# Kernel tuning notes

Measured on AMD Instinct MI355X. Metric: run time of the kernel, lower is better.

Reference implementation:

```python
import jax, jax.numpy as jnp
import numpy as np

EMB = 192
HEADS = 6
WIN = (8, 8)
N = WIN[0] * WIN[1]  # 64
B_ = 2048
NW = 1024  # mask windows per image; B_ % NW == 0


def _relative_position_index():
    coords_h = np.arange(WIN[0])
    coords_w = np.arange(WIN[1])
    coords = np.stack(np.meshgrid(coords_h, coords_w, indexing='ij'))  # (2,Wh,Ww)
    cf = coords.reshape(2, -1)
    rel = cf[:, :, None] - cf[:, None, :]  # (2,N,N)
    rel = rel.transpose(1, 2, 0)
    rel[:, :, 0] += WIN[0] - 1
    rel[:, :, 1] += WIN[1] - 1
    rel[:, :, 0] *= 2 * WIN[1] - 1
    return rel.sum(-1).astype(np.int32)  # (N,N)


def setup_inputs() -> dict:
    key = jax.random.key(0)
    ks = jax.random.split(key, 12)
    num_bias = (2 * WIN[0] - 1) * (2 * WIN[1] - 1)  # 225
    s = 0.02
    return {
        'q': jax.random.normal(ks[0], (B_, N, EMB), jnp.float32),
        'k': jax.random.normal(ks[1], (B_, N, EMB), jnp.float32),
        'v': jax.random.normal(ks[2], (B_, N, EMB), jnp.float32),
        'mask': jax.random.normal(ks[3], (NW, N, N), jnp.float32),
        'Wq': jax.random.normal(ks[4], (EMB, EMB), jnp.float32) * s,
        'bq': jnp.zeros((EMB,), jnp.float32),
        'Wk': jax.random.normal(ks[5], (EMB, EMB), jnp.float32) * s,
        'bk': jnp.zeros((EMB,), jnp.float32),
        'Wv': jax.random.normal(ks[6], (EMB, EMB), jnp.float32) * s,
        'bv': jnp.zeros((EMB,), jnp.float32),
        'Wp': jax.random.normal(ks[7], (EMB, EMB), jnp.float32) * s,
        'bp': jnp.zeros((EMB,), jnp.float32),
        'bias_table': jax.random.normal(ks[8], (num_bias, HEADS), jnp.float32) * s,
        'rel_index': jnp.asarray(_relative_position_index()),
    }


def reference(q, k, v, mask, Wq, bq, Wk, bk, Wv, bv, Wp, bp, bias_table, rel_index):
    head_dim = EMB // HEADS
    scale = head_dim ** -0.5

    def split_heads(x):
        # (B_,N,C) -> (B_,H,N,D)
        return x.reshape(B_, N, HEADS, head_dim).transpose(0, 2, 1, 3)

    qh = split_heads(q @ Wq + bq) * scale
    kh = split_heads(k @ Wk + bk)
    vh = split_heads(v @ Wv + bv)

    attn = jnp.einsum('bhnd,bhmd->bhnm', qh, kh)  # (B_,H,N,N)

    # gathered relative position bias: (N,N,H) -> (H,N,N)
    rel_bias = bias_table[rel_index.reshape(-1)].reshape(N, N, HEADS).transpose(2, 0, 1)
    attn = attn + rel_bias[None]

    # mask add: reshape to (B, nW, H, N, N) and broadcast mask over batch/heads
    nW = mask.shape[0]
    attn = attn.reshape(-1, nW, HEADS, N, N) + mask[None, :, None]
    attn = attn.reshape(-1, HEADS, N, N)
    attn = jax.nn.softmax(attn, axis=-1)

    x = jnp.einsum('bhnm,bhmd->bhnd', attn, vh)  # (B_,H,N,D)
    x = x.transpose(0, 2, 1, 3).reshape(B_, N, EMB)
    x = x @ Wp + bp
    return (x, attn)
```

## Files before the change

kernel.cpp:

```cpp
#include <hip/hip_runtime.h>
#include <hip/hip_bf16.h>

typedef __attribute__((ext_vector_type(8))) short   bf16x8;
typedef __attribute__((ext_vector_type(4))) float   f32x4;
typedef unsigned short u16;

#define NTOK 64
#define CEMB 192
#define NH   6
#define ROWB 384
#define VROWB 128

__device__ __forceinline__ u16 f2b(float f) {
  unsigned u = __float_as_uint(f);
  unsigned r = (u + 0x7fffu + ((u >> 16) & 1u)) >> 16;
  return (u16)r;
}

__device__ __forceinline__ unsigned cvtpk(float lo, float hi) {
  unsigned r;
  asm("v_cvt_pk_bf16_f32 %0, %1, %2" : "=v"(r) : "v"(lo), "v"(hi));
  return r;
}

__device__ __forceinline__ int swz(int row, int colbyte) {
  return colbyte ^ ((((row >> 3) ^ row) & 7) << 4);
}

__global__ void prep_kernel(const float* __restrict__ Wq, const float* __restrict__ Wk,
                            const float* __restrict__ Wv, const float* __restrict__ Wp,
                            const float* __restrict__ btab, const int* __restrict__ ridx,
                            u16* __restrict__ WT, float* __restrict__ rb) {
  int idx = blockIdx.x * 256 + threadIdx.x;
  if (idx < 4 * 36864) {
    int m = idx / 36864;
    int e = idx - m * 36864;
    int n = e / CEMB;
    int k = e - n * CEMB;
    const float* W = (m == 0) ? Wq : (m == 1) ? Wk : (m == 2) ? Wv : Wp;
    WT[idx] = f2b(W[k * CEMB + n]);
  } else {
    int i2 = idx - 4 * 36864;
    if (i2 < NH * 4096) {
      int h = i2 >> 12;
      int ij = i2 & 4095;
      rb[i2] = btab[ridx[ij] * NH + h];
    }
  }
}

__global__ __launch_bounds__(512, 4)
void wattn_kernel(const float* __restrict__ qg, const float* __restrict__ kg,
                  const float* __restrict__ vg, const float* __restrict__ maskg,
                  const float* __restrict__ bq, const float* __restrict__ bk,
                  const float* __restrict__ bv, const float* __restrict__ bp,
                  const u16* __restrict__ WT, const float* __restrict__ rb,
                  float* __restrict__ xout, float* __restrict__ attn_out) {
  __shared__ __align__(16) char smem[81920];
  char* sQ = smem;
  char* sK = smem + 24576;
  char* sV = smem + 49152;
  const int tid  = threadIdx.x;
  const int wave = tid >> 6;
  const int lane = tid & 63;
  const int l15  = lane & 15;
  const int lhi  = lane >> 4;
  char* sP = smem + 73728 + wave * 1024;
  const int b = blockIdx.x;
  const float scale = 0.17677669529663687f;

  {
    const size_t base = (size_t)b * NTOK * CEMB;
    #pragma unroll
    for (int m = 0; m < 3; ++m) {
      const float* src = (m == 0 ? qg : m == 1 ? kg : vg) + base;
      char* dst = (m == 0 ? sQ : m == 1 ? sK : sV);
      #pragma unroll
      for (int it = 0; it < 6; ++it) {
        int fi  = it * 512 + tid;
        int row = fi / 48;
        int ce  = (fi - row * 48) * 4;
        const float4 v4 = reinterpret_cast<const float4*>(src)[fi];
        uint2 w;
        w.x = cvtpk(v4.x, v4.y);
        w.y = cvtpk(v4.z, v4.w);
        *reinterpret_cast<uint2*>(dst + row * ROWB + swz(row, ce * 2)) = w;
      }
    }
  }
  __syncthreads();

  #pragma unroll
  for (int m = 0; m < 3; ++m) {
    const char* Xs = (m == 0) ? sQ : (m == 1) ? sK : sV;
    const float* bias = (m == 0) ? bq : (m == 1) ? bk : bv;
    f32x4 acc[2][4];
    #pragma unroll
    for (int si = 0; si < 2; ++si) {
      int strip = wave + si * 8;
      if (strip < 12) {
        const u16* Wt = WT + m * 36864 + (strip * 16 + l15) * CEMB + lhi * 8;
        #pragma unroll
        for (int rt = 0; rt < 4; ++rt) { f32x4 z = {0.f,0.f,0.f,0.f}; acc[si][rt] = z; }
        #pragma unroll
        for (int ks = 0; ks < 6; ++ks) {
          bf16x8 bw = *reinterpret_cast<const bf16x8*>(Wt + ks * 32);
          #pragma unroll
          for (int rt = 0; rt < 4; ++rt) {
            int row = rt * 16 + l15;
            bf16x8 ax = *reinterpret_cast<const bf16x8*>(Xs + row * ROWB + swz(row, ks * 64 + lhi * 16));
            acc[si][rt] = __builtin_amdgcn_mfma_f32_16x16x32_bf16(ax, bw, acc[si][rt], 0, 0, 0);
          }
        }
      }
    }
    __syncthreads();
    #pragma unroll
    for (int si = 0; si < 2; ++si) {
      int strip = wave + si * 8;
      if (strip < 12) {
        int c = strip * 16 + l15;
        float bval = bias[c];
        if (m == 0) {
          #pragma unroll
          for (int rt = 0; rt < 4; ++rt)
            #pragma unroll
            for (int r = 0; r < 4; ++r) {
              int row = rt * 16 + lhi * 4 + r;
              *reinterpret_cast<u16*>(sQ + row * ROWB + swz(row, c * 2)) = f2b((acc[si][rt][r] + bval) * scale);
            }
        } else if (m == 1) {
          #pragma unroll
          for (int rt = 0; rt < 4; ++rt)
            #pragma unroll
            for (int r = 0; r < 4; ++r) {
              int row = rt * 16 + lhi * 4 + r;
              *reinterpret_cast<u16*>(sK + row * ROWB + swz(row, c * 2)) = f2b(acc[si][rt][r] + bval);
            }
        } else {
          #pragma unroll
          for (int rt = 0; rt < 4; ++rt) {
            int t0 = rt * 16 + lhi * 4;
            uint2 w;
            w.x = cvtpk(acc[si][rt][0] + bval, acc[si][rt][1] + bval);
            w.y = cvtpk(acc[si][rt][2] + bval, acc[si][rt][3] + bval);
            *reinterpret_cast<uint2*>(sV + c * VROWB + swz(c, t0 * 2)) = w;
          }
        }
      }
    }
  }
  __syncthreads();

  const float* maskw = maskg + (size_t)(b & 1023) * 4096;
  const int rt   = wave & 3;
  const int irow = rt * 16 + lhi * 4;

  const float* mkp = maskw + irow * 64 + l15;
  float mkv[4][4];
  #pragma unroll
  for (int ct = 0; ct < 4; ++ct)
    #pragma unroll
    for (int r = 0; r < 4; ++r)
      mkv[ct][r] = mkp[r * 64 + ct * 16];

  #pragma unroll
  for (int ui = 0; ui < 3; ++ui) {
    int u = wave + ui * 8;
    int h = u >> 2;

    const float* rbp = rb + h * 4096 + irow * 64 + l15;
    float rbv[4][4];
    #pragma unroll
    for (int ct = 0; ct < 4; ++ct)
      #pragma unroll
      for (int r = 0; r < 4; ++r)
        rbv[ct][r] = rbp[r * 64 + ct * 16];

    int qrow = rt * 16 + l15;
    bf16x8 aq = *reinterpret_cast<const bf16x8*>(sQ + qrow * ROWB + swz(qrow, h * 64 + lhi * 16));
    f32x4 sv[4];
    #pragma unroll
    for (int ct = 0; ct < 4; ++ct) {
      int krow = ct * 16 + l15;
      bf16x8 bkf = *reinterpret_cast<const bf16x8*>(sK + krow * ROWB + swz(krow, h * 64 + lhi * 16));
      f32x4 z = {0.f, 0.f, 0.f, 0.f};
      sv[ct] = __builtin_amdgcn_mfma_f32_16x16x32_bf16(aq, bkf, z, 0, 0, 0);
    }

    float lg[4][4];
    #pragma unroll
    for (int ct = 0; ct < 4; ++ct)
      #pragma unroll
      for (int r = 0; r < 4; ++r)
        lg[ct][r] = sv[ct][r] + rbv[ct][r] + mkv[ct][r];

    float pr[4][4];
    #pragma unroll
    for (int r = 0; r < 4; ++r) {
      float mx = fmaxf(fmaxf(lg[0][r], lg[1][r]), fmaxf(lg[2][r], lg[3][r]));
      mx = fmaxf(mx, __shfl_xor(mx, 1));
      mx = fmaxf(mx, __shfl_xor(mx, 2));
      mx = fmaxf(mx, __shfl_xor(mx, 4));
      mx = fmaxf(mx, __shfl_xor(mx, 8));
      float e0 = __expf(lg[0][r] - mx), e1 = __expf(lg[1][r] - mx);
      float e2 = __expf(lg[2][r] - mx), e3 = __expf(lg[3][r] - mx);
      float sum = e0 + e1 + e2 + e3;
      sum += __shfl_xor(sum, 1);
      sum += __shfl_xor(sum, 2);
      sum += __shfl_xor(sum, 4);
      sum += __shfl_xor(sum, 8);
      float inv = 1.0f / sum;
      pr[0][r] = e0 * inv; pr[1][r] = e1 * inv; pr[2][r] = e2 * inv; pr[3][r] = e3 * inv;
    }

    float* ap = attn_out + (((size_t)b * NH + h) * NTOK + irow) * NTOK;
    #pragma unroll
    for (int ct = 0; ct < 4; ++ct)
      #pragma unroll
      for (int r = 0; r < 4; ++r)
        ap[r * 64 + ct * 16 + l15] = pr[ct][r];

    f32x4 xa[2];
    { f32x4 z = {0.f, 0.f, 0.f, 0.f}; xa[0] = z; xa[1] = z; }
    #pragma unroll
    for (int ks = 0; ks < 2; ++ks) {
      #pragma unroll
      for (int c = 0; c < 2; ++c)
        #pragma unroll
        for (int r = 0; r < 4; ++r) {
          int col  = c * 16 + l15;
          int kgp  = col >> 3;
          int j    = col & 7;
          int prow = lhi * 4 + r;
          *reinterpret_cast<u16*>(sP + ((kgp * 16 + prow) * 8 + j) * 2) = f2b(pr[ks * 2 + c][r]);
        }
      bf16x8 apf = *reinterpret_cast<const bf16x8*>(sP + lane * 16);
      #pragma unroll
      for (int ctv = 0; ctv < 2; ++ctv) {
        int vrow = h * 32 + ctv * 16 + l15;
        bf16x8 bvf = *reinterpret_cast<const bf16x8*>(sV + vrow * VROWB + swz(vrow, ks * 64 + lhi * 16));
        xa[ctv] = __builtin_amdgcn_mfma_f32_16x16x32_bf16(apf, bvf, xa[ctv], 0, 0, 0);
      }
    }

    #pragma unroll
    for (int ctv = 0; ctv < 2; ++ctv)
      #pragma unroll
      for (int r = 0; r < 4; ++r) {
        int xrow = rt * 16 + lhi * 4 + r;
        int xcol = h * 32 + ctv * 16 + l15;
        *reinterpret_cast<u16*>(sQ + xrow * ROWB + swz(xrow, xcol * 2)) = f2b(xa[ctv][r]);
      }
  }
  __syncthreads();

  #pragma unroll
  for (int ui = 0; ui < 3; ++ui) {
    int u2 = wave + ui * 8;
    int ct = u2 % 12;
    int rh = u2 / 12;
    const u16* Wt = WT + 3 * 36864 + (ct * 16 + l15) * CEMB + lhi * 8;
    f32x4 oa[2];
    { f32x4 z = {0.f, 0.f, 0.f, 0.f}; oa[0] = z; oa[1] = z; }
    #pragma unroll
    for (int ks = 0; ks < 6; ++ks) {
      bf16x8 bw = *reinterpret_cast<const bf16x8*>(Wt + ks * 32);
      #pragma unroll
      for (int rr = 0; rr < 2; ++rr) {
        int xrow = rh * 32 + rr * 16 + l15;
        bf16x8 ax = *reinterpret_cast<const bf16x8*>(sQ + xrow * ROWB + swz(xrow, ks * 64 + lhi * 16));
        oa[rr] = __builtin_amdgcn_mfma_f32_16x16x32_bf16(ax, bw, oa[rr], 0, 0, 0);
      }
    }
    float bias = bp[ct * 16 + l15];
    #pragma unroll
    for (int rr = 0; rr < 2; ++rr)
      #pragma unroll
      for (int r = 0; r < 4; ++r)
        xout[((size_t)b * NTOK + rh * 32 + rr * 16 + lhi * 4 + r) * CEMB + ct * 16 + l15] = oa[rr][r] + bias;
  }
}

extern "C" void kernel_launch(void* const* d_in, const int* in_sizes, int n_in,
                              void* d_out, int out_size, void* d_ws, size_t ws_size,
                              hipStream_t stream) {
  const float* q    = (const float*)d_in[0];
  const float* k    = (const float*)d_in[1];
  const float* v    = (const float*)d_in[2];
  const float* mask = (const float*)d_in[3];
  const float* Wq   = (const float*)d_in[4];
  const float* bq   = (const float*)d_in[5];
  const float* Wk   = (const float*)d_in[6];
  const float* bk   = (const float*)d_in[7];
  const float* Wv   = (const float*)d_in[8];
  const float* bv   = (const float*)d_in[9];
  const float* Wp   = (const float*)d_in[10];
  const float* bp   = (const float*)d_in[11];
  const float* btab = (const float*)d_in[12];
  const int*   ridx = (const int*)d_in[13];

  u16*   WT = (u16*)d_ws;
  float* rb = (float*)((char*)d_ws + 4 * 36864 * 2);

  float* xout = (float*)d_out;
  float* attn = xout + (size_t)2048 * NTOK * CEMB;

  prep_kernel<<<672, 256, 0, stream>>>(Wq, Wk, Wv, Wp, btab, ridx, WT, rb);
  wattn_kernel<<<2048, 512, 0, stream>>>(q, k, v, mask, bq, bk, bv, bp, WT, rb, xout, attn);
}
```

Measured before the change: 203.9 us.

## Transpose QK^T MFMA output so each lane holds a row segment for vectorized softmax I/O

Swaps the MFMA operand order so the score tile comes out transposed: each lane now holds four consecutive columns of one query row instead of one column of four rows. This lets the mask, relative bias and attention-probability stores use 16-byte float4 accesses in place of scalar strided ones. The row softmax reductions drop from four shuffles per row to two shuffles across lane groups. The P staging into LDS uses packed bf16 conversion and 8-byte stores. The attention output write, about 200MB, dominates memory traffic, so wider stores should help coalescing. The P layout in LDS must still match what the PV MFMA expects.

Measured after the change: 214.0 us. 4.9% more time.

```diff
diff --git a/kernel.cpp b/kernel.cpp
--- a/kernel.cpp
+++ b/kernel.cpp
@@ -154,30 +154,24 @@
 
   const float* maskw = maskg + (size_t)(b & 1023) * 4096;
   const int rt   = wave & 3;
+  const int qrow = rt * 16 + l15;
   const int irow = rt * 16 + lhi * 4;
 
-  const float* mkp = maskw + irow * 64 + l15;
-  float mkv[4][4];
+  f32x4 mk4[4];
   #pragma unroll
   for (int ct = 0; ct < 4; ++ct)
-    #pragma unroll
-    for (int r = 0; r < 4; ++r)
-      mkv[ct][r] = mkp[r * 64 + ct * 16];
+    mk4[ct] = *reinterpret_cast<const f32x4*>(maskw + qrow * 64 + ct * 16 + lhi * 4);
 
   #pragma unroll
   for (int ui = 0; ui < 3; ++ui) {
     int u = wave + ui * 8;
     int h = u >> 2;
 
-    const float* rbp = rb + h * 4096 + irow * 64 + l15;
-    float rbv[4][4];
+    f32x4 rb4[4];
     #pragma unroll
     for (int ct = 0; ct < 4; ++ct)
-      #pragma unroll
-      for (int r = 0; r < 4; ++r)
-        rbv[ct][r] = rbp[r * 64 + ct * 16];
-
-    int qrow = rt * 16 + l15;
+      rb4[ct] = *reinterpret_cast<const f32x4*>(rb + h * 4096 + qrow * 64 + ct * 16 + lhi * 4);
+
     bf16x8 aq = *reinterpret_cast<const bf16x8*>(sQ + qrow * ROWB + swz(qrow, h * 64 + lhi * 16));
     f32x4 sv[4];
     #pragma unroll
@@ -185,7 +179,7 @@
       int krow = ct * 16 + l15;
       bf16x8 bkf = *reinterpret_cast<const bf16x8*>(sK + krow * ROWB + swz(krow, h * 64 + lhi * 16));
       f32x4 z = {0.f, 0.f, 0.f, 0.f};
-      sv[ct] = __builtin_amdgcn_mfma_f32_16x16x32_bf16(aq, bkf, z, 0, 0, 0);
+      sv[ct] = __builtin_amdgcn_mfma_f32_16x16x32_bf16(bkf, aq, z, 0, 0, 0);
     }
 
     float lg[4][4];
@@ -193,48 +187,56 @@
     for (int ct = 0; ct < 4; ++ct)
       #pragma unroll
       for (int r = 0; r < 4; ++r)
-        lg[ct][r] = sv[ct][r] + rbv[ct][r] + mkv[ct][r];
+        lg[ct][r] = sv[ct][r] + rb4[ct][r] + mk4[ct][r];
+
+    float mx = fmaxf(fmaxf(fmaxf(lg[0][0], lg[0][1]), fmaxf(lg[0][2], lg[0][3])),
+                     fmaxf(fmaxf(lg[1][0], lg[1][1]), fmaxf(lg[1][2], lg[1][3])));
+    mx = fmaxf(mx, fmaxf(fmaxf(fmaxf(lg[2][0], lg[2][1]), fmaxf(lg[2][2], lg[2][3])),
+                         fmaxf(fmaxf(lg[3][0], lg[3][1]), fmaxf(lg[3][2], lg[3][3]))));
+    mx = fmaxf(mx, __shfl_xor(mx, 16));
+    mx = fmaxf(mx, __shfl_xor(mx, 32));
+
+    float e[4][4];
+    float sum = 0.f;
+    #pragma unroll
+    for (int ct = 0; ct < 4; ++ct)
+      #pragma unroll
+      for (int r = 0; r < 4; ++r) {
+        e[ct][r] = __expf(lg[ct][r] - mx);
+        sum += e[ct][r];
+      }
+    sum += __shfl_xor(sum, 16);
+    sum += __shfl_xor(sum, 32);
+    float inv = 1.0f / sum;
 
     float pr[4][4];
     #pragma unroll
-    for (int r = 0; r < 4; ++r) {
-      float mx = fmaxf(fmaxf(lg[0][r], lg[1][r]), fmaxf(lg[2][r], lg[3][r]));
-      mx = fmaxf(mx, __shfl_xor(mx, 1));
-      mx = fmaxf(mx, __shfl_xor(mx, 2));
-      mx = fmaxf(mx, __shfl_xor(mx, 4));
-      mx = fmaxf(mx, __shfl_xor(mx, 8));
-      float e0 = __expf(lg[0][r] - mx), e1 = __expf(lg[1][r] - mx);
-      float e2 = __expf(lg[2][r] - mx), e3 = __expf(lg[3][r] - mx);
-      float sum = e0 + e1 + e2 + e3;
-      sum += __shfl_xor(sum, 1);
-      sum += __shfl_xor(sum, 2);
-      sum += __shfl_xor(sum, 4);
-      sum += __shfl_xor(sum, 8);
-      float inv = 1.0f / sum;
-      pr[0][r] = e0 * inv; pr[1][r] = e1 * inv; pr[2][r] = e2 * inv; pr[3][r] = e3 * inv;
-    }
-
-    float* ap = attn_out + (((size_t)b * NH + h) * NTOK + irow) * NTOK;
-    #pragma unroll
     for (int ct = 0; ct < 4; ++ct)
       #pragma unroll
       for (int r = 0; r < 4; ++r)
-        ap[r * 64 + ct * 16 + l15] = pr[ct][r];
+        pr[ct][r] = e[ct][r] * inv;
+
+    float* ap = attn_out + ((size_t)b * NH + h) * 4096 + qrow * 64;
+    #pragma unroll
+    for (int ct = 0; ct < 4; ++ct) {
+      f32x4 p4;
+      p4[0] = pr[ct][0]; p4[1] = pr[ct][1]; p4[2] = pr[ct][2]; p4[3] = pr[ct][3];
+      *reinterpret_cast<f32x4*>(ap + ct * 16 + lhi * 4) = p4;
+    }
 
     f32x4 xa[2];
     { f32x4 z = {0.f, 0.f, 0.f, 0.f}; xa[0] = z; xa[1] = z; }
     #pragma unroll
     for (int ks = 0; ks < 2; ++ks) {
       #pragma unroll
-      for (int c = 0; c < 2; ++c)
-        #pragma unroll
-        for (int r = 0; r < 4; ++r) {
-          int col  = c * 16 + l15;
-          int kgp  = col >> 3;
-          int j    = col & 7;
-          int prow = lhi * 4 + r;
-          *reinterpret_cast<u16*>(sP + ((kgp * 16 + prow) * 8 + j) * 2) = f2b(pr[ks * 2 + c][r]);
-        }
+      for (int c = 0; c < 2; ++c) {
+        int ct = ks * 2 + c;
+        int kg = c * 2 + (lhi >> 1);
+        uint2 w;
+        w.x = cvtpk(pr[ct][0], pr[ct][1]);
+        w.y = cvtpk(pr[ct][2], pr[ct][3]);
+        *reinterpret_cast<uint2*>(sP + (kg * 16 + l15) * 16 + (lhi & 1) * 8) = w;
+      }
       bf16x8 apf = *reinterpret_cast<const bf16x8*>(sP + lane * 16);
       #pragma unroll
       for (int ctv = 0; ctv < 2; ++ctv) {
@@ -248,7 +250,7 @@
     for (int ctv = 0; ctv < 2; ++ctv)
       #pragma unroll
       for (int r = 0; r < 4; ++r) {
-        int xrow = rt * 16 + lhi * 4 + r;
+        int xrow = irow + r;
         int xcol = h * 32 + ctv * 16 + l15;
         *reinterpret_cast<u16*>(sQ + xrow * ROWB + swz(xrow, xcol * 2)) = f2b(xa[ctv][r]);
       }
```
